# Kernel tuning notes

Measured on AMD Instinct MI355X. Metric: run time of the kernel, lower is better.

The kernel has to match this reference:

```python
import jax, jax.numpy as jnp
import numpy as np

N_NODES = 100000
N_EDGES = 1600000
D_IN = 128
D_HID = 128
D_OUT = 64
N_LAYERS = 3
BN_EPS = 1e-5


def _mlp_block(h, W1, b1, g, be, W2, b2):
    # PyG MLP([c_in, h, h]): Linear -> BatchNorm -> ReLU -> Linear (plain last)
    h = h @ W1 + b1                      # [N, h]
    mu = jnp.mean(h, axis=0)
    var = jnp.var(h, axis=0)             # biased var, BN training-mode stats
    h = (h - mu) * jax.lax.rsqrt(var + BN_EPS) * g + be
    h = jax.nn.relu(h)
    return h @ W2 + b2


def setup_inputs() -> dict:
    key = jax.random.key(0)
    ks = jax.random.split(key, 16)
    s_in = 1.0 / np.sqrt(D_IN)
    s_h = 1.0 / np.sqrt(D_HID)
    x = jax.random.normal(ks[0], (N_NODES, D_IN), dtype=jnp.float32)
    edge_index = jax.random.randint(ks[1], (2, N_EDGES), 0, N_NODES, dtype=jnp.int64)
    return {
        "x": x,
        "edge_index": edge_index,
        # stacked per-conv MLP params (all layers are 128->128->128)
        "W1": jax.random.normal(ks[2], (N_LAYERS, D_IN, D_HID), jnp.float32) * s_in,
        "b1": jnp.zeros((N_LAYERS, D_HID), jnp.float32),
        "g1": jnp.ones((N_LAYERS, D_HID), jnp.float32),
        "be1": jnp.zeros((N_LAYERS, D_HID), jnp.float32),
        "W2": jax.random.normal(ks[3], (N_LAYERS, D_HID, D_HID), jnp.float32) * s_h,
        "b2": jnp.zeros((N_LAYERS, D_HID), jnp.float32),
        # final MLP([h, h, out])
        "fW1": jax.random.normal(ks[4], (D_HID, D_HID), jnp.float32) * s_h,
        "fb1": jnp.zeros((D_HID,), jnp.float32),
        "fg1": jnp.ones((D_HID,), jnp.float32),
        "fbe1": jnp.zeros((D_HID,), jnp.float32),
        "fW2": jax.random.normal(ks[5], (D_HID, D_OUT), jnp.float32) * s_h,
        "fb2": jnp.zeros((D_OUT,), jnp.float32),
    }


def reference(x, edge_index, W1, b1, g1, be1, W2, b2, fW1, fb1, fg1, fbe1, fW2, fb2):
    src, dst = edge_index[0], edge_index[1]
    for l in range(N_LAYERS):
        # GINConv, eps=0: nn((1+eps)*x + sum_{j->i} x_j)
        aggr = jax.ops.segment_sum(x[src], dst, num_segments=N_NODES)  # [N, d]
        h = x + aggr
        x = jax.nn.relu(_mlp_block(h, W1[l], b1[l], g1[l], be1[l], W2[l], b2[l]))
    # final MLP (dropout=0.5 is identity in eval mode)
    return _mlp_block(x, fW1, fb1, fg1, fbe1, fW2, fb2)
```

## Files before the change

### kernel.cpp

```cpp
#include <hip/hip_runtime.h>

#define NN 100000
#define NE 1600000
#define DD 128
#define CAP 56
#define NGROUP 256

static __device__ __forceinline__ unsigned short f2b(float f) {
  unsigned int x = __float_as_uint(f);
  unsigned int r = x + 0x7fffu + ((x >> 16) & 1u);
  return (unsigned short)(r >> 16);
}
static __device__ __forceinline__ float b2f(unsigned short u) {
  return __uint_as_float(((unsigned int)u) << 16);
}

typedef __attribute__((ext_vector_type(8))) short short8;
typedef __attribute__((ext_vector_type(4))) float f32x4;

union V8 {
  uint4 u4;
  short8 s8;
  unsigned short us[8];
};

__global__ void detect_k(const int* __restrict__ ei, int* __restrict__ flag) {
  int v = ei[2 * threadIdx.x + 1];
  unsigned long long b = __ballot(v != 0);
  if (threadIdx.x == 0) *flag = (b == 0ull) ? 1 : 0;
}

__global__ __launch_bounds__(256) void cast_k(const float* __restrict__ x,
                                              unsigned short* __restrict__ x16) {
  size_t i = ((size_t)blockIdx.x * 256 + threadIdx.x) * 8;
  f32x4 a = *(const f32x4*)(x + i);
  f32x4 b = *(const f32x4*)(x + i + 4);
  V8 v;
#pragma unroll
  for (int j = 0; j < 4; ++j) {
    v.us[j] = f2b(a[j]);
    v.us[4 + j] = f2b(b[j]);
  }
  *(uint4*)(x16 + i) = v.u4;
}

__global__ __launch_bounds__(256) void pack_k(const int* __restrict__ ei,
                                              int2* __restrict__ packed,
                                              int* __restrict__ cnt,
                                              float* __restrict__ stats,
                                              const int* __restrict__ flag) {
  const int mode = *flag;
  const int gid = blockIdx.x * 256 + threadIdx.x;
  int s, d;
  if (mode) {
    s = ((const int2*)ei)[gid].x;
    d = ((const int2*)ei)[(size_t)NE + gid].x;
  } else {
    s = ei[gid];
    d = ei[NE + gid];
  }
  packed[gid] = make_int2(s, d);
  if (gid < NN) cnt[gid] = 0;
  if (gid < 1024) stats[gid] = 0.f;
}

__global__ __launch_bounds__(256) void scatter_k(const int2* __restrict__ packed,
                                                 int* __restrict__ cnt,
                                                 int* __restrict__ csr) {
  const int r = blockIdx.x & 7;
  const int g = blockIdx.x >> 3;
  const int lo = r * (NN / 8), hi = lo + (NN / 8);
  for (int e = g * 256 + threadIdx.x; e < NE; e += NGROUP * 256) {
    int2 sd = packed[e];
    if (sd.y >= lo && sd.y < hi) {
      int c = atomicAdd(&cnt[sd.y], 1);
      if (c < CAP) csr[(size_t)sd.y * CAP + c] = sd.x;
    }
  }
}

__global__ __launch_bounds__(256) void wprep_k(const float* __restrict__ W1,
                                               const float* __restrict__ W2,
                                               const float* __restrict__ fW1,
                                               const float* __restrict__ fW2,
                                               unsigned short* __restrict__ wt) {
  int b = blockIdx.x;
  const float* src;
  int moff, N;
  if (b < 192) {
    int m = b >> 6;
    src = W1 + m * 16384;
    moff = m * 16384;
    N = 128;
    b &= 63;
  } else if (b < 384) {
    int m = (b - 192) >> 6;
    src = W2 + m * 16384;
    moff = (3 + m) * 16384;
    N = 128;
    b = (b - 192) & 63;
  } else if (b < 448) {
    src = fW1;
    moff = 6 * 16384;
    N = 128;
    b -= 384;
  } else {
    src = fW2;
    moff = 7 * 16384;
    N = 64;
    b -= 448;
  }
  int idx = b * 256 + threadIdx.x;
  int n = idx >> 7, k = idx & 127;
  if (n < N) wt[moff + idx] = f2b(src[(size_t)k * N + n]);
}

__global__ __launch_bounds__(256) void gather_k(const int* __restrict__ cnt,
                                                const int* __restrict__ csr,
                                                const unsigned short* __restrict__ x16,
                                                unsigned short* __restrict__ h16) {
  const int node = blockIdx.x * 16 + (threadIdx.x >> 4);
  const int l = threadIdx.x & 15;
  const int beg = node * CAP;
  const int end = beg + cnt[node];
  V8 v;
  v.u4 = *(const uint4*)(x16 + (size_t)node * DD + l * 8);
  float a0[8], a1[8], a2[8], a3[8];
#pragma unroll
  for (int j = 0; j < 8; ++j) {
    a0[j] = b2f(v.us[j]);
    a1[j] = 0.f;
    a2[j] = 0.f;
    a3[j] = 0.f;
  }
  int p = beg;
  for (; p + 4 <= end; p += 4) {
    const int s0 = csr[p], s1 = csr[p + 1], s2 = csr[p + 2], s3 = csr[p + 3];
    V8 w0, w1, w2, w3;
    w0.u4 = *(const uint4*)(x16 + (size_t)s0 * DD + l * 8);
    w1.u4 = *(const uint4*)(x16 + (size_t)s1 * DD + l * 8);
    w2.u4 = *(const uint4*)(x16 + (size_t)s2 * DD + l * 8);
    w3.u4 = *(const uint4*)(x16 + (size_t)s3 * DD + l * 8);
#pragma unroll
    for (int j = 0; j < 8; ++j) {
      a0[j] += b2f(w0.us[j]);
      a1[j] += b2f(w1.us[j]);
      a2[j] += b2f(w2.us[j]);
      a3[j] += b2f(w3.us[j]);
    }
  }
  for (; p < end; ++p) {
    const int s0 = csr[p];
    V8 w0;
    w0.u4 = *(const uint4*)(x16 + (size_t)s0 * DD + l * 8);
#pragma unroll
    for (int j = 0; j < 8; ++j) a0[j] += b2f(w0.us[j]);
  }
  V8 o;
#pragma unroll
  for (int j = 0; j < 8; ++j) o.us[j] = f2b((a0[j] + a1[j]) + (a2[j] + a3[j]));
  *(uint4*)(h16 + (size_t)node * DD + l * 8) = o.u4;
}

template <int AMODE, int NCOLS, int EPI, int STATS>
__global__ __launch_bounds__(512) void gemm_k(const unsigned short* __restrict__ Aptr,
                                              const unsigned short* __restrict__ wT,
                                              const float* __restrict__ bias,
                                              const float* __restrict__ bn_stats,
                                              const float* __restrict__ gamma,
                                              const float* __restrict__ beta,
                                              void* __restrict__ Cptr,
                                              float* __restrict__ stats_out) {
  __shared__ unsigned short bT[NCOLS][136];
  __shared__ float biasS[NCOLS];
  __shared__ float scS[128];
  __shared__ float shS[128];
  __shared__ float sS[NCOLS];
  __shared__ float s2S[NCOLS];
  const int tid = threadIdx.x;
  const int wv = tid >> 6;
  const int lane = tid & 63;
  const int l16 = lane & 15;
  const int quad = lane >> 4;
  const int arow = blockIdx.x * 128 + wv * 16 + l16;
  const bool rv = arow < NN;

  V8 afr[4];
#pragma unroll
  for (int kc = 0; kc < 4; ++kc) {
    if (rv) {
      afr[kc].u4 = *(const uint4*)(Aptr + (size_t)arow * DD + kc * 32 + quad * 8);
    } else {
      afr[kc].u4 = make_uint4(0u, 0u, 0u, 0u);
    }
  }

  for (int i = tid; i < NCOLS * 16; i += 512) {
    int n = i >> 4, k8 = (i & 15) << 3;
    *(uint4*)&bT[n][k8] = *(const uint4*)(wT + n * 128 + k8);
  }
  if (tid < NCOLS) biasS[tid] = bias[tid];
  if (AMODE == 2 && tid < 128) {
    const float inv_n = 1.0f / (float)NN;
    float mu = bn_stats[tid] * inv_n;
    float var = bn_stats[128 + tid] * inv_n - mu * mu;
    float sc = gamma[tid] * rsqrtf(var + 1e-5f);
    scS[tid] = sc;
    shS[tid] = beta[tid] - mu * sc;
  }
  if (STATS && tid < NCOLS) {
    sS[tid] = 0.f;
    s2S[tid] = 0.f;
  }
  __syncthreads();

  f32x4 acc[NCOLS / 16];
#pragma unroll
  for (int nt = 0; nt < NCOLS / 16; ++nt) acc[nt] = (f32x4)(0.0f);

#pragma unroll
  for (int kc = 0; kc < 4; ++kc) {
    const int k0 = kc * 32 + quad * 8;
    V8 af = afr[kc];
    if (AMODE == 2) {
#pragma unroll
      for (int j = 0; j < 8; ++j) {
        float f = fmaf(b2f(af.us[j]), scS[k0 + j], shS[k0 + j]);
        af.us[j] = f2b(fmaxf(f, 0.0f));
      }
    }
#pragma unroll
    for (int nt = 0; nt < NCOLS / 16; ++nt) {
      V8 bf;
      bf.u4 = *(const uint4*)&bT[nt * 16 + l16][k0];
      acc[nt] = __builtin_amdgcn_mfma_f32_16x16x32_bf16(af.s8, bf.s8, acc[nt], 0, 0, 0);
    }
  }

  const int r0 = blockIdx.x * 128 + wv * 16 + quad * 4;
#pragma unroll
  for (int nt = 0; nt < NCOLS / 16; ++nt) {
    const int col = nt * 16 + l16;
    const float bv = biasS[col];
    float s = 0.f, s2 = 0.f;
#pragma unroll
    for (int i = 0; i < 4; ++i) {
      const int r = r0 + i;
      if (r < NN) {
        float v = acc[nt][i] + bv;
        if (EPI == 1) v = fmaxf(v, 0.0f);
        if (EPI == 2) {
          ((float*)Cptr)[(size_t)r * NCOLS + col] = v;
        } else {
          unsigned short us = f2b(v);
          ((unsigned short*)Cptr)[(size_t)r * NCOLS + col] = us;
          if (STATS) {
            float vr = b2f(us);
            s += vr;
            s2 += vr * vr;
          }
        }
      }
    }
    if (STATS) {
      s += __shfl_xor(s, 16);
      s += __shfl_xor(s, 32);
      s2 += __shfl_xor(s2, 16);
      s2 += __shfl_xor(s2, 32);
      if (quad == 0) {
        atomicAdd(&sS[col], s);
        atomicAdd(&s2S[col], s2);
      }
    }
  }
  if (STATS) {
    __syncthreads();
    if (tid < NCOLS) {
      atomicAdd(&stats_out[tid], sS[tid]);
      atomicAdd(&stats_out[128 + tid], s2S[tid]);
    }
  }
}

extern "C" void kernel_launch(void* const* d_in, const int* in_sizes, int n_in,
                              void* d_out, int out_size, void* d_ws, size_t ws_size,
                              hipStream_t stream) {
  const float* x = (const float*)d_in[0];
  const int* ei = (const int*)d_in[1];
  const float* W1 = (const float*)d_in[2];
  const float* b1 = (const float*)d_in[3];
  const float* g1 = (const float*)d_in[4];
  const float* be1 = (const float*)d_in[5];
  const float* W2 = (const float*)d_in[6];
  const float* b2 = (const float*)d_in[7];
  const float* fW1 = (const float*)d_in[8];
  const float* fb1 = (const float*)d_in[9];
  const float* fg1 = (const float*)d_in[10];
  const float* fbe1 = (const float*)d_in[11];
  const float* fW2 = (const float*)d_in[12];
  const float* fb2 = (const float*)d_in[13];

  char* ws = (char*)d_ws;
  unsigned short* x16 = (unsigned short*)ws;
  unsigned short* h16 = (unsigned short*)(ws + (size_t)25600000);
  unsigned short* t16 = (unsigned short*)(ws + (size_t)51200000);
  int2* packed = (int2*)t16;
  int* csr = (int*)(ws + (size_t)76800000);
  int* cnt = (int*)(ws + (size_t)99200000);
  float* stats = (float*)(ws + (size_t)99600000);
  int* flag = (int*)(ws + (size_t)99604096);
  unsigned short* wt = (unsigned short*)(ws + (size_t)99605504);

  const int vecBlocks = (NN * DD) / (256 * 8);
  const int gemmBlocks = (NN + 127) / 128;
  const int edgeBlocks = NE / 256;
  const int filtBlocks = NGROUP * 8;
  const int nodeBlocks = NN / 16;

  detect_k<<<1, 64, 0, stream>>>(ei, flag);
  cast_k<<<vecBlocks, 256, 0, stream>>>(x, x16);
  pack_k<<<edgeBlocks, 256, 0, stream>>>(ei, packed, cnt, stats, flag);
  wprep_k<<<480, 256, 0, stream>>>(W1, W2, fW1, fW2, wt);
  scatter_k<<<filtBlocks, 256, 0, stream>>>(packed, cnt, csr);

  for (int l = 0; l < 3; ++l) {
    gather_k<<<nodeBlocks, 256, 0, stream>>>(cnt, csr, x16, h16);
    gemm_k<1, 128, 0, 1><<<gemmBlocks, 512, 0, stream>>>(
        h16, wt + (size_t)l * 16384, b1 + l * 128, nullptr, nullptr, nullptr,
        t16, stats + 256 * l);
    gemm_k<2, 128, 1, 0><<<gemmBlocks, 512, 0, stream>>>(
        t16, wt + (size_t)(3 + l) * 16384, b2 + l * 128, stats + 256 * l,
        g1 + l * 128, be1 + l * 128, x16, nullptr);
  }

  gemm_k<1, 128, 0, 1><<<gemmBlocks, 512, 0, stream>>>(
      x16, wt + (size_t)6 * 16384, fb1, nullptr, nullptr, nullptr, t16,
      stats + 768);
  gemm_k<2, 64, 2, 0><<<gemmBlocks, 512, 0, stream>>>(
      t16, wt + (size_t)7 * 16384, fb2, stats + 768, fg1, fbe1, (float*)d_out,
      nullptr);
}
```

Baseline: 595.4 us.

## Pre-bucket edges by destination range in pack to avoid filtered rescans

Pack now sorts each edge into one of 8 destination-range buckets, using per-block shared counters and one global atomic per bucket per block. Scatter then reads only its own bucket instead of every block scanning all edges and filtering by range. This removes the 8x redundant reads of the packed edge list in scatter. The cost is extra atomics and scattered writes in pack, plus a fixed bucket capacity that silently drops edges if a bucket overflows.

```diff
diff --git a/kernel.cpp b/kernel.cpp
--- a/kernel.cpp
+++ b/kernel.cpp
@@ -4,7 +4,8 @@
 #define NE 1600000
 #define DD 128
 #define CAP 56
-#define NGROUP 256
+#define BCAP 208896
+#define SBLK 128
 
 static __device__ __forceinline__ unsigned short f2b(float f) {
   unsigned int x = __float_as_uint(f);
@@ -24,10 +25,12 @@
   unsigned short us[8];
 };
 
-__global__ void detect_k(const int* __restrict__ ei, int* __restrict__ flag) {
+__global__ void detect_k(const int* __restrict__ ei, int* __restrict__ flag,
+                         int* __restrict__ bcur) {
   int v = ei[2 * threadIdx.x + 1];
   unsigned long long b = __ballot(v != 0);
   if (threadIdx.x == 0) *flag = (b == 0ull) ? 1 : 0;
+  if (threadIdx.x < 8) bcur[threadIdx.x] = 0;
 }
 
 __global__ __launch_bounds__(256) void cast_k(const float* __restrict__ x,
@@ -45,12 +48,18 @@
 }
 
 __global__ __launch_bounds__(256) void pack_k(const int* __restrict__ ei,
-                                              int2* __restrict__ packed,
+                                              int2* __restrict__ buckets,
+                                              int* __restrict__ bcur,
                                               int* __restrict__ cnt,
                                               float* __restrict__ stats,
                                               const int* __restrict__ flag) {
+  __shared__ int lcnt[8];
+  __shared__ int lbase[8];
+  const int tid = threadIdx.x;
+  if (tid < 8) lcnt[tid] = 0;
+  __syncthreads();
   const int mode = *flag;
-  const int gid = blockIdx.x * 256 + threadIdx.x;
+  const int gid = blockIdx.x * 256 + tid;
   int s, d;
   if (mode) {
     s = ((const int2*)ei)[gid].x;
@@ -59,23 +68,29 @@
     s = ei[gid];
     d = ei[NE + gid];
   }
-  packed[gid] = make_int2(s, d);
+  const int r = d / (NN / 8);
+  const int slot = atomicAdd(&lcnt[r], 1);
+  __syncthreads();
+  if (tid < 8) lbase[tid] = atomicAdd(&bcur[tid], lcnt[tid]);
+  __syncthreads();
+  const int idx = lbase[r] + slot;
+  if (idx < BCAP) buckets[(size_t)r * BCAP + idx] = make_int2(s, d);
   if (gid < NN) cnt[gid] = 0;
   if (gid < 1024) stats[gid] = 0.f;
 }
 
-__global__ __launch_bounds__(256) void scatter_k(const int2* __restrict__ packed,
+__global__ __launch_bounds__(256) void scatter_k(const int2* __restrict__ buckets,
+                                                 const int* __restrict__ bcur,
                                                  int* __restrict__ cnt,
                                                  int* __restrict__ csr) {
   const int r = blockIdx.x & 7;
   const int g = blockIdx.x >> 3;
-  const int lo = r * (NN / 8), hi = lo + (NN / 8);
-  for (int e = g * 256 + threadIdx.x; e < NE; e += NGROUP * 256) {
-    int2 sd = packed[e];
-    if (sd.y >= lo && sd.y < hi) {
-      int c = atomicAdd(&cnt[sd.y], 1);
-      if (c < CAP) csr[(size_t)sd.y * CAP + c] = sd.x;
-    }
+  const int nb = min(bcur[r], BCAP);
+  const int2* bk = buckets + (size_t)r * BCAP;
+  for (int e = g * 256 + threadIdx.x; e < nb; e += SBLK * 256) {
+    int2 sd = bk[e];
+    int c = atomicAdd(&cnt[sd.y], 1);
+    if (c < CAP) csr[(size_t)sd.y * CAP + c] = sd.x;
   }
 }
 
@@ -304,24 +319,25 @@
   unsigned short* x16 = (unsigned short*)ws;
   unsigned short* h16 = (unsigned short*)(ws + (size_t)25600000);
   unsigned short* t16 = (unsigned short*)(ws + (size_t)51200000);
-  int2* packed = (int2*)t16;
+  int2* buckets = (int2*)t16;
   int* csr = (int*)(ws + (size_t)76800000);
   int* cnt = (int*)(ws + (size_t)99200000);
   float* stats = (float*)(ws + (size_t)99600000);
   int* flag = (int*)(ws + (size_t)99604096);
+  int* bcur = (int*)(ws + (size_t)99604224);
   unsigned short* wt = (unsigned short*)(ws + (size_t)99605504);
 
   const int vecBlocks = (NN * DD) / (256 * 8);
   const int gemmBlocks = (NN + 127) / 128;
   const int edgeBlocks = NE / 256;
-  const int filtBlocks = NGROUP * 8;
+  const int scatBlocks = SBLK * 8;
   const int nodeBlocks = NN / 16;
 
-  detect_k<<<1, 64, 0, stream>>>(ei, flag);
+  detect_k<<<1, 64, 0, stream>>>(ei, flag, bcur);
   cast_k<<<vecBlocks, 256, 0, stream>>>(x, x16);
-  pack_k<<<edgeBlocks, 256, 0, stream>>>(ei, packed, cnt, stats, flag);
+  pack_k<<<edgeBlocks, 256, 0, stream>>>(ei, buckets, bcur, cnt, stats, flag);
   wprep_k<<<480, 256, 0, stream>>>(W1, W2, fW1, fW2, wt);
-  scatter_k<<<filtBlocks, 256, 0, stream>>>(packed, cnt, csr);
+  scatter_k<<<scatBlocks, 256, 0, stream>>>(buckets, bcur, cnt, csr);
 
   for (int l = 0; l < 3; ++l) {
     gather_k<<<nodeBlocks, 256, 0, stream>>>(cnt, csr, x16, h16);
```

Result: slower. 664.3 us (+11.6%).
